# Kernel optimization log

Measured on AMD Instinct MI355X. Metric: run time of the kernel, lower is better.

The kernel has to match this reference:

```python
import jax, jax.numpy as jnp
import numpy as np

# --- dims from Mamba3Config defaults ---
D_MODEL = 768
D_STATE = 192
EXPAND = 2
HEADDIM = 64
D_INNER = EXPAND * D_MODEL        # 1536
NHEADS = D_INNER // HEADDIM       # 24
NGROUPS = 1
NROT = int(D_STATE * 0.5)         # rope_fraction=0.5 -> 96 rotated state dims
NPAIR = NROT // 2                 # 48
A_FLOOR = 1e-4
DT_MIN, DT_MAX = 1e-3, 0.1
EPS = 1e-6
BATCH, SEQ = 1, 1024
D_INPROJ = 2 * D_INNER + 2 * NGROUPS * D_STATE + NHEADS  # 3480


def zcrms(x, scale):
    # Zero-centered RMSNorm: (1 + scale) * RMSNorm(x)
    y = x * jax.lax.rsqrt(jnp.mean(x * x, axis=-1, keepdims=True) + EPS)
    return y * (1.0 + scale)


def _rotate(v, cos, sin):
    # Rotate first NROT state dims in pairs by angle phi (cos/sin: [B,L,H,NPAIR]).
    vr = v[..., :NROT].reshape(v.shape[:-1] + (NPAIR, 2))
    v0, v1 = vr[..., 0], vr[..., 1]
    rot = jnp.stack([v0 * cos - v1 * sin, v0 * sin + v1 * cos], axis=-1)
    return jnp.concatenate([rot.reshape(v.shape[:-1] + (NROT,)), v[..., NROT:]], axis=-1)


def _mamba3(h, W_in, dt_bias, A_log, omega, D, norm_weight, W_out):
    Bsz, L, _ = h.shape
    zxbcdt = h @ W_in  # [B,L,3480]
    z = zxbcdt[..., :D_INNER]
    u = zxbcdt[..., D_INNER:2 * D_INNER].reshape(Bsz, L, NHEADS, HEADDIM)
    Bm = zxbcdt[..., 2 * D_INNER:2 * D_INNER + D_STATE]              # [B,L,N] (ngroups=1)
    Cm = zxbcdt[..., 2 * D_INNER + D_STATE:2 * D_INNER + 2 * D_STATE]
    dt_raw = zxbcdt[..., -NHEADS:]

    dt = jax.nn.softplus(dt_raw + dt_bias)        # [B,L,H]
    A = -(jnp.exp(A_log) + A_FLOOR)               # [H], strictly negative (A_floor)
    a = jnp.exp(dt * A)                           # per-step real decay [B,L,H]

    # Complex-state machinery: data-dependent rotation angle phi_t = cumsum(dt)*omega.
    # y_t = sum_s C e^{i th (Phi_t - Phi_s)} B_s u_s  ==  (C rotated by +Phi_t) . scan of (B rotated by -Phi_s) u_s
    phi = jnp.cumsum(dt, axis=1)[..., None] * omega  # [B,L,H,NPAIR]
    cosp, sinp = jnp.cos(phi), jnp.sin(phi)
    Bh = jnp.broadcast_to(Bm[:, :, None, :], (Bsz, L, NHEADS, D_STATE))
    Ch = jnp.broadcast_to(Cm[:, :, None, :], (Bsz, L, NHEADS, D_STATE))
    Brot = _rotate(Bh, cosp, -sinp)  # e^{-i Phi_s} B_s
    Crot = _rotate(Ch, cosp, sinp)   # e^{+i Phi_t} C_t

    halfdt = 0.5 * dt  # trapezoid weights
    # shifted (t-1) sequences for the trapezoid's previous endpoint
    Bprev = jnp.concatenate([jnp.zeros_like(Brot[:, :1]), Brot[:, :-1]], axis=1)
    uprev = jnp.concatenate([jnp.zeros_like(u[:, :1]), u[:, :-1]], axis=1)

    def step(h_prev, inp):
        a_t, hd_t, B_t, Bp_t, C_t, u_t, up_t = inp
        Bu = jnp.einsum('bhn,bhp->bhpn', B_t, u_t)
        Bu_prev = jnp.einsum('bhn,bhp->bhpn', Bp_t, up_t)
        # exp-trapezoid discretization:
        # h_t = e^{dt A} h_{t-1} + (dt/2) B_t u_t + e^{dt A} (dt/2) B_{t-1} u_{t-1}
        hs = (a_t[..., None, None] * h_prev
              + hd_t[..., None, None] * Bu
              + (a_t * hd_t)[..., None, None] * Bu_prev)
        y = jnp.einsum('bhpn,bhn->bhp', hs, C_t)
        return hs, y

    h0 = jnp.zeros((Bsz, NHEADS, HEADDIM, D_STATE), dtype=h.dtype)
    xs = tuple(jnp.moveaxis(t, 1, 0) for t in (a, halfdt, Brot, Bprev, Crot, u, uprev))
    _, ys = jax.lax.scan(step, h0, xs)
    y = jnp.moveaxis(ys, 0, 1)  # [B,L,H,P]

    y = y + D[None, None, :, None] * u  # skip connection
    y = y.reshape(Bsz, L, D_INNER)
    g = y * jax.nn.silu(z)              # gated
    g = g * jax.lax.rsqrt(jnp.mean(g * g, axis=-1, keepdims=True) + EPS) * norm_weight
    return g @ W_out


def setup_inputs() -> dict:
    key = jax.random.key(0)
    ks = jax.random.split(key, 8)
    x = jax.random.normal(ks[0], (BATCH, SEQ, D_MODEL), jnp.float32)
    W_in = jax.random.normal(ks[1], (D_MODEL, D_INPROJ), jnp.float32) * 0.02
    # dt_bias init so softplus(bias) is in [dt_min, dt_max]
    dtv = jnp.exp(jax.random.uniform(ks[2], (NHEADS,)) * (np.log(DT_MAX) - np.log(DT_MIN)) + np.log(DT_MIN))
    dt_bias = dtv + jnp.log(-jnp.expm1(-dtv))
    A_log = jnp.log(jax.random.uniform(ks[3], (NHEADS,), minval=1.0, maxval=16.0))
    omega = jnp.tile((10000.0 ** (-jnp.arange(NPAIR, dtype=jnp.float32) / NPAIR))[None, :], (NHEADS, 1))
    Dp = 1.0 + 0.1 * jax.random.normal(ks[4], (NHEADS,), jnp.float32)
    norm_weight = jnp.ones((D_INNER,), jnp.float32)
    W_out = jax.random.normal(ks[5], (D_INNER, D_MODEL), jnp.float32) * 0.02
    pre_scale = jnp.zeros((D_MODEL,), jnp.float32)
    post_scale = jnp.zeros((D_MODEL,), jnp.float32)
    return dict(x=x, pre_scale=pre_scale, W_in=W_in, dt_bias=dt_bias, A_log=A_log,
                omega=omega, D=Dp, norm_weight=norm_weight, W_out=W_out, post_scale=post_scale)


def reference(x, pre_scale, W_in, dt_bias, A_log, omega, D, norm_weight, W_out, post_scale):
    residual = x
    h = zcrms(x, pre_scale)
    y = _mamba3(h, W_in, dt_bias, A_log, omega, D, norm_weight, W_out)
    y = zcrms(y, post_scale)
    return residual + y  # dropout=0.0
```

## Files before the change

### kernel.cpp

```cpp
#include <hip/hip_runtime.h>
#include <cstdint>

#define L_SEQ   1024
#define DMODEL  768
#define DINNER  1536
#define NHEADS  24
#define HEADDIM 64
#define DSTATE  192
#define NPAIR   48
#define DPROJ   3480
#define NPADJ   3584
#define NCHUNK  16
#define QCH     64
#define EPSF    1e-6f

typedef __attribute__((ext_vector_type(8))) short short8;
typedef __attribute__((ext_vector_type(4))) float f32x4;

__device__ __forceinline__ unsigned short f2bf(float x) {
  union { float f; uint32_t u; } v; v.f = x;
  uint32_t r = (v.u + 0x7FFFu + ((v.u >> 16) & 1u)) >> 16;
  return (unsigned short)r;
}
__device__ __forceinline__ float bf2f(unsigned short b) {
  union { float f; uint32_t u; } v; v.u = ((uint32_t)b) << 16;
  return v.f;
}

__device__ __forceinline__ float blockReduceSum256(float v, float* red) {
#pragma unroll
  for (int m = 32; m; m >>= 1) v += __shfl_xor(v, m, 64);
  int wid = threadIdx.x >> 6, lane = threadIdx.x & 63;
  if (lane == 0) red[wid] = v;
  __syncthreads();
  float s = red[0] + red[1] + red[2] + red[3];
  __syncthreads();
  return s;
}

__global__ __launch_bounds__(256) void k_cvtw(const float* __restrict__ W,
                                              unsigned short* __restrict__ Wh,
                                              int K, int N, int Npad) {
  __shared__ float tile[32][33];
  int n0 = blockIdx.x * 32, k0 = blockIdx.y * 32;
  int tr = threadIdx.x >> 3, tc4 = (threadIdx.x & 7) << 2;
  const float* wp = W + (size_t)(k0 + tr) * N + n0 + tc4;
  float4 v = make_float4(0.f, 0.f, 0.f, 0.f);
  if (n0 + tc4 + 3 < N) {
    v = *(const float4*)wp;
  } else {
    if (n0 + tc4     < N) v.x = wp[0];
    if (n0 + tc4 + 1 < N) v.y = wp[1];
    if (n0 + tc4 + 2 < N) v.z = wp[2];
    if (n0 + tc4 + 3 < N) v.w = wp[3];
  }
  tile[tr][tc4 + 0] = v.x; tile[tr][tc4 + 1] = v.y;
  tile[tr][tc4 + 2] = v.z; tile[tr][tc4 + 3] = v.w;
  __syncthreads();
  ushort4 oh;
  oh.x = f2bf(tile[tc4 + 0][tr]);
  oh.y = f2bf(tile[tc4 + 1][tr]);
  oh.z = f2bf(tile[tc4 + 2][tr]);
  oh.w = f2bf(tile[tc4 + 3][tr]);
  *(ushort4*)&Wh[(size_t)(n0 + tr) * K + k0 + tc4] = oh;
}

__global__ __launch_bounds__(256) void k_prenorm_dt(const float* __restrict__ x,
                                                    const float* __restrict__ pre_scale,
                                                    const float* __restrict__ W_in,
                                                    unsigned short* __restrict__ hb,
                                                    float* __restrict__ dtr) {
  __shared__ float hs[DMODEL];
  __shared__ float red[4];
  __shared__ float part[NHEADS][8];
  int l = blockIdx.x, tid = threadIdx.x;
  const float* xr = x + (size_t)l * DMODEL;
  float v[3]; float ss = 0.f;
#pragma unroll
  for (int k = 0; k < 3; ++k) { v[k] = xr[tid + k * 256]; ss += v[k] * v[k]; }
  ss = blockReduceSum256(ss, red);
  float r = rsqrtf(ss * (1.f / DMODEL) + EPSF);
#pragma unroll
  for (int k = 0; k < 3; ++k) {
    int i = tid + k * 256;
    float hv = v[k] * r * (1.f + pre_scale[i]);
    hs[i] = hv;
    hb[(size_t)l * DMODEL + i] = f2bf(hv);
  }
  __syncthreads();
  if (tid < 192) {
    int hh = tid >> 3, seg = tid & 7;
    float s = 0.f;
    int k0 = seg * 96;
#pragma unroll 4
    for (int k = k0; k < k0 + 96; ++k)
      s = fmaf(hs[k], W_in[(size_t)k * DPROJ + 3456 + hh], s);
    part[hh][seg] = s;
  }
  __syncthreads();
  if (tid < NHEADS) {
    float s = 0.f;
#pragma unroll
    for (int q = 0; q < 8; ++q) s += part[tid][q];
    dtr[(size_t)l * NHEADS + tid] = s;
  }
}

template<int BM, int BN, int TM, int TN>
__global__ __launch_bounds__(256) void k_gemm_bf16(
    const unsigned short* __restrict__ A,
    const unsigned short* __restrict__ Bt,
    float* __restrict__ C,
    int N, int K, int ldc) {
  __shared__ unsigned short As[BM * 32];
  __shared__ unsigned short Bs[BN * 32];
  const int tid = threadIdx.x;
  const int lane = tid & 63, w = tid >> 6;
  const int wm = (w >> 1) * (TM * 16), wn = (w & 1) * (TN * 16);
  const int bm = blockIdx.y * BM, bn = blockIdx.x * BN;
  const int r15 = lane & 15, kg = lane >> 4;
  f32x4 acc[TM][TN] = {};
  for (int k0 = 0; k0 < K; k0 += 32) {
    __syncthreads();
#pragma unroll
    for (int ch = tid; ch < BM * 4; ch += 256) {
      int r = ch >> 2, kq = (ch & 3) << 3;
      *(short8*)&As[r * 32 + kq] = *(const short8*)&A[(size_t)(bm + r) * K + k0 + kq];
    }
#pragma unroll
    for (int ch = tid; ch < BN * 4; ch += 256) {
      int r = ch >> 2, kq = (ch & 3) << 3;
      *(short8*)&Bs[r * 32 + kq] = *(const short8*)&Bt[(size_t)(bn + r) * K + k0 + kq];
    }
    __syncthreads();
    short8 af[TM], bfr[TN];
#pragma unroll
    for (int i = 0; i < TM; ++i)
      af[i] = *(const short8*)&As[(wm + i * 16 + r15) * 32 + kg * 8];
#pragma unroll
    for (int j = 0; j < TN; ++j)
      bfr[j] = *(const short8*)&Bs[(wn + j * 16 + r15) * 32 + kg * 8];
#pragma unroll
    for (int i = 0; i < TM; ++i)
#pragma unroll
      for (int j = 0; j < TN; ++j)
        acc[i][j] = __builtin_amdgcn_mfma_f32_16x16x32_bf16(af[i], bfr[j], acc[i][j], 0, 0, 0);
  }
  const int crow = bm + wm + (lane >> 4) * 4;
  const int ccol = bn + wn + r15;
#pragma unroll
  for (int i = 0; i < TM; ++i)
#pragma unroll
    for (int j = 0; j < TN; ++j) {
      int col = ccol + j * 16;
      if (col < N) {
        float* cp = C + (size_t)(crow + i * 16) * ldc + col;
#pragma unroll
        for (int r = 0; r < 4; ++r) cp[(size_t)r * ldc] = acc[i][j][r];
      }
    }
}

__global__ __launch_bounds__(256) void k_dtscan(const float* __restrict__ dtr,
                                                const float* __restrict__ dt_bias,
                                                const float* __restrict__ A_log,
                                                float* __restrict__ halfdt,
                                                float* __restrict__ cfac,
                                                float* __restrict__ cumdt,
                                                float* __restrict__ cumD) {
  __shared__ float sdt[L_SEQ];
  __shared__ float wsum[4];
  int hh = blockIdx.x, tid = threadIdx.x;
  int lane = tid & 63, wid = tid >> 6;
  float bias = dt_bias[hh];
  float Ah = -(expf(A_log[hh]) + 1e-4f);
  int l0 = tid * 4;
  float d[4], e[4];
#pragma unroll
  for (int k = 0; k < 4; ++k) {
    float draw = dtr[(size_t)(l0 + k) * NHEADS + hh] + bias;
    d[k] = (draw > 20.f) ? draw : log1pf(expf(draw));
    sdt[l0 + k] = d[k];
  }
  e[0] = d[0]; e[1] = e[0] + d[1]; e[2] = e[1] + d[2]; e[3] = e[2] + d[3];
  float tot = e[3];
  float s = tot;
#pragma unroll
  for (int off = 1; off < 64; off <<= 1) {
    float n = __shfl_up(s, off, 64);
    if (lane >= off) s += n;
  }
  if (lane == 63) wsum[wid] = s;
  __syncthreads();
  float woff = 0.f;
#pragma unroll
  for (int q = 0; q < 4; ++q) woff += (q < wid) ? wsum[q] : 0.f;
  float excl = woff + s - tot;
  float cd0 = excl + e[0], cd1 = excl + e[1], cd2 = excl + e[2], cd3 = excl + e[3];
  float dnext3 = (l0 + 3 < L_SEQ - 1) ? sdt[l0 + 4] : 0.f;
  float4 o_hd = make_float4(0.5f * d[0], 0.5f * d[1], 0.5f * d[2], 0.5f * d[3]);
  float4 o_cf = make_float4(0.5f * (d[0] + d[1]), 0.5f * (d[1] + d[2]),
                            0.5f * (d[2] + d[3]), 0.5f * (d[3] + dnext3));
  float4 o_cd = make_float4(cd0, cd1, cd2, cd3);
  float4 o_cD = make_float4(Ah * cd0, Ah * cd1, Ah * cd2, Ah * cd3);
  size_t idx = (size_t)hh * L_SEQ + l0;
  *(float4*)&halfdt[idx] = o_hd;
  *(float4*)&cfac[idx]   = o_cf;
  *(float4*)&cumdt[idx]  = o_cd;
  *(float4*)&cumD[idx]   = o_cD;
}

__global__ __launch_bounds__(256) void k_rotate(const float* __restrict__ zx,
                                                const float* __restrict__ cumdt,
                                                const float* __restrict__ omega,
                                                unsigned short* __restrict__ Brot,
                                                unsigned short* __restrict__ Crot,
                                                float* __restrict__ U) {
  int l = blockIdx.x, tid = threadIdx.x;
  const float* row = zx + (size_t)l * DPROJ;
  for (int i = tid; i < 384; i += 256) {
    float4 v = *(const float4*)(row + 1536 + i * 4);
    int hh = i >> 4;
    int p = (i & 15) << 2;
    *(float4*)&U[((size_t)(hh * L_SEQ + l)) * HEADDIM + p] = v;
  }
  for (int i = tid; i < NHEADS * 96; i += 256) {
    int hh = i / 96, j = i - hh * 96;
    int n = 2 * j;
    float b0 = row[3072 + n], b1 = row[3072 + n + 1];
    float c0 = row[3264 + n], c1 = row[3264 + n + 1];
    size_t base = ((size_t)(hh * L_SEQ + l)) * DSTATE + n;
    float br0 = b0, br1 = b1, cr0 = c0, cr1 = c1;
    if (j < NPAIR) {
      float ph = cumdt[hh * L_SEQ + l] * omega[hh * NPAIR + j];
      float sp, cp;
      sincosf(ph, &sp, &cp);
      br0 =  b0 * cp + b1 * sp;
      br1 = -b0 * sp + b1 * cp;
      cr0 =  c0 * cp - c1 * sp;
      cr1 =  c0 * sp + c1 * cp;
    }
    ushort2 bo, co;
    bo.x = f2bf(br0); bo.y = f2bf(br1);
    co.x = f2bf(cr0); co.y = f2bf(cr1);
    *(ushort2*)&Brot[base] = bo;
    *(ushort2*)&Crot[base] = co;
  }
}

__global__ __launch_bounds__(256) void k_chunkX(const unsigned short* __restrict__ Brot,
                                                const float* __restrict__ U,
                                                const float* __restrict__ cumD,
                                                const float* __restrict__ cfac,
                                                float* __restrict__ X) {
  const int c = blockIdx.x, hh = blockIdx.y;
  const int tid = threadIdx.x;
  const size_t hl = (size_t)hh * L_SEQ;
  const int l0 = c * QCH;
  __shared__ float Bs[QCH][DSTATE];
  __shared__ float su[QCH][HEADDIM];
  for (int i = tid; i < QCH * 48; i += 256) {
    int m = i / 48, q = i - m * 48;
    ushort4 bv = *(const ushort4*)&Brot[(hl + l0 + m) * DSTATE + (q << 2)];
    Bs[m][(q << 2) + 0] = bf2f(bv.x);
    Bs[m][(q << 2) + 1] = bf2f(bv.y);
    Bs[m][(q << 2) + 2] = bf2f(bv.z);
    Bs[m][(q << 2) + 3] = bf2f(bv.w);
  }
  float dlast = cumD[hl + l0 + QCH - 1];
  for (int i = tid; i < QCH * 16; i += 256) {
    int m = i >> 4, q = i & 15;
    float s = expf(dlast - cumD[hl + l0 + m]) * cfac[hl + l0 + m];
    float4 v = *(const float4*)&U[(hl + l0 + m) * HEADDIM + (q << 2)];
    v.x *= s; v.y *= s; v.z *= s; v.w *= s;
    *(float4*)&su[m][q << 2] = v;
  }
  __syncthreads();
  const int ngrp = tid & 15, pgrp = tid >> 4;
  const int n0 = ngrp * 12, p0 = pgrp << 2;
  float acc[12][4] = {};
  for (int m = 0; m < QCH; ++m) {
    const float4 uv = *(const float4*)&su[m][p0];
    const float4 b0 = *(const float4*)&Bs[m][n0];
    const float4 b1 = *(const float4*)&Bs[m][n0 + 4];
    const float4 b2 = *(const float4*)&Bs[m][n0 + 8];
    float u4[4] = {uv.x, uv.y, uv.z, uv.w};
    float bb[12] = {b0.x, b0.y, b0.z, b0.w, b1.x, b1.y, b1.z, b1.w, b2.x, b2.y, b2.z, b2.w};
#pragma unroll
    for (int j = 0; j < 12; ++j)
#pragma unroll
      for (int i = 0; i < 4; ++i) acc[j][i] = fmaf(bb[j], u4[i], acc[j][i]);
  }
  const size_t obase = ((size_t)(hh * NCHUNK + c)) * (HEADDIM * DSTATE);
#pragma unroll
  for (int i = 0; i < 4; ++i)
#pragma unroll
    for (int j4 = 0; j4 < 3; ++j4)
      *(float4*)&X[obase + (size_t)(p0 + i) * DSTATE + n0 + j4 * 4] =
          make_float4(acc[j4 * 4 + 0][i], acc[j4 * 4 + 1][i], acc[j4 * 4 + 2][i], acc[j4 * 4 + 3][i]);
}

__global__ __launch_bounds__(256) void k_statepass(const float* __restrict__ X,
                                                   const float* __restrict__ cumD,
                                                   unsigned short* __restrict__ Hs) {
  int hh = blockIdx.x >> 3, part = blockIdx.x & 7;
  int tid = threadIdx.x;
  const size_t hl = (size_t)hh * L_SEQ;
  float Hc[6] = {0.f, 0.f, 0.f, 0.f, 0.f, 0.f};
  for (int c = 0; c < NCHUNK; ++c) {
    float r = 1.f;
    if (c > 0) r = expf(cumD[hl + c * QCH + QCH - 1] - cumD[hl + c * QCH - 1]);
    size_t base = ((size_t)(hh * NCHUNK + c)) * (HEADDIM * DSTATE) + part * 1536 + tid;
#pragma unroll
    for (int k = 0; k < 6; ++k) {
      Hs[base + k * 256] = f2bf(Hc[k]);
      Hc[k] = fmaf(r, Hc[k], X[base + k * 256]);
    }
  }
}

#define YP 104
#define SP 72
__global__ __launch_bounds__(256) void k_yout_mfma(
    const unsigned short* __restrict__ Brot, const unsigned short* __restrict__ Crot,
    const float* __restrict__ U,             const unsigned short* __restrict__ Hs,
    const float* __restrict__ cumD, const float* __restrict__ cfac,
    const float* __restrict__ halfdt, const float* __restrict__ Dvec,
    float* __restrict__ Yout) {
  const int c = blockIdx.x, hh = blockIdx.y;
  const int tid = threadIdx.x;
  const int lane = tid & 63, w = tid >> 6;
  const int wr = w >> 1, wc = w & 1;
  const int r15 = lane & 15, kg = lane >> 4;
  const int l0 = c * QCH;
  const size_t hl = (size_t)hh * L_SEQ;

  __shared__ unsigned short Cs[64][YP];
  __shared__ unsigned short Bs[64][YP];
  __shared__ unsigned short Ss[64][SP];
  __shared__ unsigned short Ut[64][SP];
  __shared__ float Dc[64], cfs[64], hds[64];

  if (tid < 64) {
    Dc[tid]  = cumD[hl + l0 + tid];
    cfs[tid] = cfac[hl + l0 + tid];
    hds[tid] = halfdt[hl + l0 + tid];
  }
  for (int idx = tid; idx < 64 * 64; idx += 256) {
    int m = idx >> 6, p = idx & 63;
    Ut[p][m] = f2bf(U[(hl + l0 + m) * HEADDIM + p]);
  }

  f32x4 accS[2][2] = {};
  for (int half = 0; half < 2; ++half) {
    __syncthreads();
    for (int idx = tid; idx < 64 * 12; idx += 256) {
      int t = idx / 12, q = (idx % 12) << 3;
      *(short8*)&Cs[t][q] = *(const short8*)&Crot[(hl + l0 + t) * DSTATE + 96 * half + q];
      *(short8*)&Bs[t][q] = *(const short8*)&Brot[(hl + l0 + t) * DSTATE + 96 * half + q];
    }
    __syncthreads();
#pragma unroll
    for (int kk = 0; kk < 3; ++kk) {
      short8 af[2], bfr[2];
#pragma unroll
      for (int i = 0; i < 2; ++i)
        af[i] = *(const short8*)&Cs[wr * 32 + i * 16 + r15][kk * 32 + kg * 8];
#pragma unroll
      for (int j = 0; j < 2; ++j)
        bfr[j] = *(const short8*)&Bs[wc * 32 + j * 16 + r15][kk * 32 + kg * 8];
#pragma unroll
      for (int i = 0; i < 2; ++i)
#pragma unroll
        for (int j = 0; j < 2; ++j)
          accS[i][j] = __builtin_amdgcn_mfma_f32_16x16x32_bf16(af[i], bfr[j], accS[i][j], 0, 0, 0);
    }
  }
#pragma unroll
  for (int i = 0; i < 2; ++i)
#pragma unroll
    for (int j = 0; j < 2; ++j)
#pragma unroll
      for (int r = 0; r < 4; ++r) {
        int t = wr * 32 + i * 16 + kg * 4 + r;
        int m = wc * 32 + j * 16 + r15;
        float wgt = 0.f;
        if (m < t)       wgt = __expf(Dc[t] - Dc[m]) * cfs[m];
        else if (m == t) wgt = hds[t];
        Ss[t][m] = f2bf(accS[i][j][r] * wgt);
      }

  f32x4 accZ[2][2] = {};
  const size_t hcb = ((size_t)(hh * NCHUNK + c)) * (HEADDIM * DSTATE);
  for (int half = 0; half < 2; ++half) {
    __syncthreads();
    for (int idx = tid; idx < 64 * 12; idx += 256) {
      int t = idx / 12, q = (idx % 12) << 3;
      *(short8*)&Cs[t][q] = *(const short8*)&Crot[(hl + l0 + t) * DSTATE + 96 * half + q];
      *(short8*)&Bs[t][q] = *(const short8*)&Hs[hcb + (size_t)t * DSTATE + 96 * half + q];
    }
    __syncthreads();
#pragma unroll
    for (int kk = 0; kk < 3; ++kk) {
      short8 af[2], bfr[2];
#pragma unroll
      for (int i = 0; i < 2; ++i)
        af[i] = *(const short8*)&Cs[wr * 32 + i * 16 + r15][kk * 32 + kg * 8];
#pragma unroll
      for (int j = 0; j < 2; ++j)
        bfr[j] = *(const short8*)&Bs[wc * 32 + j * 16 + r15][kk * 32 + kg * 8];
#pragma unroll
      for (int i = 0; i < 2; ++i)
#pragma unroll
        for (int j = 0; j < 2; ++j)
          accZ[i][j] = __builtin_amdgcn_mfma_f32_16x16x32_bf16(af[i], bfr[j], accZ[i][j], 0, 0, 0);
    }
  }

  f32x4 accY[2][2] = {};
#pragma unroll
  for (int kk = 0; kk < 2; ++kk) {
    short8 af[2], bfr[2];
#pragma unroll
    for (int i = 0; i < 2; ++i)
      af[i] = *(const short8*)&Ss[wr * 32 + i * 16 + r15][kk * 32 + kg * 8];
#pragma unroll
    for (int j = 0; j < 2; ++j)
      bfr[j] = *(const short8*)&Ut[wc * 32 + j * 16 + r15][kk * 32 + kg * 8];
#pragma unroll
    for (int i = 0; i < 2; ++i)
#pragma unroll
      for (int j = 0; j < 2; ++j)
        accY[i][j] = __builtin_amdgcn_mfma_f32_16x16x32_bf16(af[i], bfr[j], accY[i][j], 0, 0, 0);
  }

  float Dbase = (c > 0) ? cumD[hl + l0 - 1] : 0.f;
  float Dh = Dvec[hh];
#pragma unroll
  for (int i = 0; i < 2; ++i)
#pragma unroll
    for (int r = 0; r < 4; ++r) {
      int t = wr * 32 + i * 16 + kg * 4 + r;
      float et = __expf(Dc[t] - Dbase);
#pragma unroll
      for (int j = 0; j < 2; ++j) {
        int p = wc * 32 + j * 16 + r15;
        float u = U[(hl + l0 + t) * HEADDIM + p];
        Yout[(size_t)(l0 + t) * DINNER + hh * HEADDIM + p] =
            accY[i][j][r] + et * accZ[i][j][r] + Dh * u;
      }
    }
}

__global__ __launch_bounds__(256) void k_gate(const float* __restrict__ Y,
                                              const float* __restrict__ zx,
                                              const float* __restrict__ nw,
                                              unsigned short* __restrict__ Gh) {
  __shared__ float gbuf[DINNER];
  __shared__ float red[4];
  int l = blockIdx.x, tid = threadIdx.x;
  float ss = 0.f;
  for (int i = tid; i < DINNER; i += 256) {
    float y = Y[(size_t)l * DINNER + i];
    float z = zx[(size_t)l * DPROJ + i];
    float g = y * z / (1.f + expf(-z));
    gbuf[i] = g;
    ss += g * g;
  }
  ss = blockReduceSum256(ss, red);
  float r = rsqrtf(ss * (1.f / DINNER) + EPSF);
  for (int i = tid; i < DINNER; i += 256)
    Gh[(size_t)l * DINNER + i] = f2bf(gbuf[i] * r * nw[i]);
}

__global__ __launch_bounds__(256) void k_final(const float* __restrict__ x,
                                               const float* __restrict__ T,
                                               const float* __restrict__ post_scale,
                                               float* __restrict__ out) {
  __shared__ float red[4];
  int l = blockIdx.x, tid = threadIdx.x;
  const float* tr = T + (size_t)l * DMODEL;
  float v[3]; float ss = 0.f;
#pragma unroll
  for (int k = 0; k < 3; ++k) { v[k] = tr[tid + k * 256]; ss += v[k] * v[k]; }
  ss = blockReduceSum256(ss, red);
  float r = rsqrtf(ss * (1.f / DMODEL) + EPSF);
#pragma unroll
  for (int k = 0; k < 3; ++k) {
    int i = tid + k * 256;
    out[(size_t)l * DMODEL + i] = x[(size_t)l * DMODEL + i] + v[k] * r * (1.f + post_scale[i]);
  }
}

extern "C" void kernel_launch(void* const* d_in, const int* in_sizes, int n_in,
                              void* d_out, int out_size, void* d_ws, size_t ws_size,
                              hipStream_t stream) {
  const float* x      = (const float*)d_in[0];
  const float* pre_s  = (const float*)d_in[1];
  const float* W_in   = (const float*)d_in[2];
  const float* dt_b   = (const float*)d_in[3];
  const float* A_log  = (const float*)d_in[4];
  const float* omega  = (const float*)d_in[5];
  const float* Dvec   = (const float*)d_in[6];
  const float* nw     = (const float*)d_in[7];
  const float* W_out  = (const float*)d_in[8];
  const float* post_s = (const float*)d_in[9];
  float* out = (float*)d_out;

  float* ws = (float*)d_ws;
  size_t off = 0;
  auto nxt = [&](size_t n) { float* p = ws + off; off += (n + 3) & ~(size_t)3; return p; };
  float* ws_zx  = nxt((size_t)L_SEQ * DPROJ);
  unsigned short* ws_hb = (unsigned short*)nxt((size_t)L_SEQ * DMODEL / 2);
  float* ws_dtr = nxt((size_t)L_SEQ * NHEADS);
  float* ws_hd  = nxt((size_t)NHEADS * L_SEQ);
  float* ws_cf  = nxt((size_t)NHEADS * L_SEQ);
  float* ws_cdt = nxt((size_t)NHEADS * L_SEQ);
  float* ws_cD  = nxt((size_t)NHEADS * L_SEQ);
  unsigned short* ws_Brb = (unsigned short*)nxt((size_t)NHEADS * L_SEQ * DSTATE / 2);
  unsigned short* ws_Crb = (unsigned short*)nxt((size_t)NHEADS * L_SEQ * DSTATE / 2);
  float* ws_U   = nxt((size_t)NHEADS * L_SEQ * HEADDIM);
  float* ws_X   = nxt((size_t)NHEADS * NCHUNK * HEADDIM * DSTATE);
  unsigned short* ws_Hsb = (unsigned short*)nxt((size_t)NHEADS * NCHUNK * HEADDIM * DSTATE / 2);
  float* ws_Y   = nxt((size_t)L_SEQ * DINNER);
  unsigned short* ws_Gh = (unsigned short*)nxt((size_t)L_SEQ * DINNER / 2);
  unsigned short* ws_W1h = (unsigned short*)ws_X;
  unsigned short* ws_W2h = ws_Brb;
  float* ws_T = ws_X;

  k_cvtw<<<dim3(NPADJ / 32, DMODEL / 32), 256, 0, stream>>>(W_in, ws_W1h, DMODEL, DPROJ, NPADJ);
  k_prenorm_dt<<<L_SEQ, 256, 0, stream>>>(x, pre_s, W_in, ws_hb, ws_dtr);
  k_gemm_bf16<128, 128, 4, 4><<<dim3(NPADJ / 128, L_SEQ / 128), 256, 0, stream>>>(
      ws_hb, ws_W1h, ws_zx, DPROJ, DMODEL, DPROJ);
  k_dtscan<<<NHEADS, 256, 0, stream>>>(ws_dtr, dt_b, A_log, ws_hd, ws_cf, ws_cdt, ws_cD);
  k_rotate<<<L_SEQ, 256, 0, stream>>>(ws_zx, ws_cdt, omega, ws_Brb, ws_Crb, ws_U);
  k_chunkX<<<dim3(NCHUNK, NHEADS), 256, 0, stream>>>(ws_Brb, ws_U, ws_cD, ws_cf, ws_X);
  k_statepass<<<NHEADS * 8, 256, 0, stream>>>(ws_X, ws_cD, ws_Hsb);
  k_yout_mfma<<<dim3(NCHUNK, NHEADS), 256, 0, stream>>>(ws_Brb, ws_Crb, ws_U, ws_Hsb, ws_cD, ws_cf, ws_hd, Dvec, ws_Y);
  k_cvtw<<<dim3(DMODEL / 32, DINNER / 32), 256, 0, stream>>>(W_out, ws_W2h, DINNER, DMODEL, DMODEL);
  k_gate<<<L_SEQ, 256, 0, stream>>>(ws_Y, ws_zx, nw, ws_Gh);
  k_gemm_bf16<64, 64, 2, 2><<<dim3(DMODEL / 64, L_SEQ / 64), 256, 0, stream>>>(
      ws_Gh, ws_W2h, ws_T, DMODEL, DINNER, DMODEL);
  k_final<<<L_SEQ, 256, 0, stream>>>(x, ws_T, post_s, out);
}
```

Before: 218.8 us.

## Merge weight conversions, prefetch GEMM tiles in registers, store U as bf16

Both weight transpose/convert kernels become one launch writing to dedicated workspace buffers, which removes a launch and the aliasing onto scratch. The bf16 GEMM now loads the next K-slice into registers while computing the current one, hiding global load latency at the cost of more registers. The first GEMM's tile shrinks to 128x64 to launch more blocks. U is stored as bf16 instead of fp32, halving its traffic in the scan kernels but losing precision on the D skip term.

```diff
diff --git a/kernel.cpp b/kernel.cpp
--- a/kernel.cpp
+++ b/kernel.cpp
@@ -38,11 +38,20 @@
   return s;
 }
 
-__global__ __launch_bounds__(256) void k_cvtw(const float* __restrict__ W,
-                                              unsigned short* __restrict__ Wh,
-                                              int K, int N, int Npad) {
+__global__ __launch_bounds__(256) void k_cvtw2(const float* __restrict__ Wa,
+                                               unsigned short* __restrict__ Wha,
+                                               const float* __restrict__ Wb,
+                                               unsigned short* __restrict__ Whb) {
   __shared__ float tile[32][33];
-  int n0 = blockIdx.x * 32, k0 = blockIdx.y * 32;
+  int b = blockIdx.x;
+  const float* W; unsigned short* Wt; int K, N, bx, by;
+  if (b < 112 * 24) {
+    W = Wa; Wt = Wha; K = DMODEL; N = DPROJ; bx = b % 112; by = b / 112;
+  } else {
+    b -= 112 * 24;
+    W = Wb; Wt = Whb; K = DINNER; N = DMODEL; bx = b % 24; by = b / 24;
+  }
+  int n0 = bx * 32, k0 = by * 32;
   int tr = threadIdx.x >> 3, tc4 = (threadIdx.x & 7) << 2;
   const float* wp = W + (size_t)(k0 + tr) * N + n0 + tc4;
   float4 v = make_float4(0.f, 0.f, 0.f, 0.f);
@@ -62,7 +71,7 @@
   oh.y = f2bf(tile[tc4 + 1][tr]);
   oh.z = f2bf(tile[tc4 + 2][tr]);
   oh.w = f2bf(tile[tc4 + 3][tr]);
-  *(ushort4*)&Wh[(size_t)(n0 + tr) * K + k0 + tc4] = oh;
+  *(ushort4*)&Wt[(size_t)(n0 + tr) * K + k0 + tc4] = oh;
 }
 
 __global__ __launch_bounds__(256) void k_prenorm_dt(const float* __restrict__ x,
@@ -112,6 +121,8 @@
     const unsigned short* __restrict__ Bt,
     float* __restrict__ C,
     int N, int K, int ldc) {
+  constexpr int AC = (BM * 4) / 256;
+  constexpr int BC = (BN * 4) / 256;
   __shared__ unsigned short As[BM * 32];
   __shared__ unsigned short Bs[BN * 32];
   const int tid = threadIdx.x;
@@ -119,20 +130,34 @@
   const int wm = (w >> 1) * (TM * 16), wn = (w & 1) * (TN * 16);
   const int bm = blockIdx.y * BM, bn = blockIdx.x * BN;
   const int r15 = lane & 15, kg = lane >> 4;
+  short8 ra[AC], rb[BC];
+  auto loadG = [&](int k0) {
+#pragma unroll
+    for (int a = 0; a < AC; ++a) {
+      int idx = tid + a * 256; int r = idx >> 2, kq = (idx & 3) << 3;
+      ra[a] = *(const short8*)&A[(size_t)(bm + r) * K + k0 + kq];
+    }
+#pragma unroll
+    for (int b = 0; b < BC; ++b) {
+      int idx = tid + b * 256; int r = idx >> 2, kq = (idx & 3) << 3;
+      rb[b] = *(const short8*)&Bt[(size_t)(bn + r) * K + k0 + kq];
+    }
+  };
   f32x4 acc[TM][TN] = {};
+  loadG(0);
   for (int k0 = 0; k0 < K; k0 += 32) {
+#pragma unroll
+    for (int a = 0; a < AC; ++a) {
+      int idx = tid + a * 256; int r = idx >> 2, kq = (idx & 3) << 3;
+      *(short8*)&As[r * 32 + kq] = ra[a];
+    }
+#pragma unroll
+    for (int b = 0; b < BC; ++b) {
+      int idx = tid + b * 256; int r = idx >> 2, kq = (idx & 3) << 3;
+      *(short8*)&Bs[r * 32 + kq] = rb[b];
+    }
     __syncthreads();
-#pragma unroll
-    for (int ch = tid; ch < BM * 4; ch += 256) {
-      int r = ch >> 2, kq = (ch & 3) << 3;
-      *(short8*)&As[r * 32 + kq] = *(const short8*)&A[(size_t)(bm + r) * K + k0 + kq];
-    }
-#pragma unroll
-    for (int ch = tid; ch < BN * 4; ch += 256) {
-      int r = ch >> 2, kq = (ch & 3) << 3;
-      *(short8*)&Bs[r * 32 + kq] = *(const short8*)&Bt[(size_t)(bn + r) * K + k0 + kq];
-    }
-    __syncthreads();
+    if (k0 + 32 < K) loadG(k0 + 32);
     short8 af[TM], bfr[TN];
 #pragma unroll
     for (int i = 0; i < TM; ++i)
@@ -145,6 +170,7 @@
 #pragma unroll
       for (int j = 0; j < TN; ++j)
         acc[i][j] = __builtin_amdgcn_mfma_f32_16x16x32_bf16(af[i], bfr[j], acc[i][j], 0, 0, 0);
+    __syncthreads();
   }
   const int crow = bm + wm + (lane >> 4) * 4;
   const int ccol = bn + wn + r15;
@@ -215,14 +241,16 @@
                                                 const float* __restrict__ omega,
                                                 unsigned short* __restrict__ Brot,
                                                 unsigned short* __restrict__ Crot,
-                                                float* __restrict__ U) {
+                                                unsigned short* __restrict__ Ub) {
   int l = blockIdx.x, tid = threadIdx.x;
   const float* row = zx + (size_t)l * DPROJ;
   for (int i = tid; i < 384; i += 256) {
     float4 v = *(const float4*)(row + 1536 + i * 4);
     int hh = i >> 4;
     int p = (i & 15) << 2;
-    *(float4*)&U[((size_t)(hh * L_SEQ + l)) * HEADDIM + p] = v;
+    ushort4 o;
+    o.x = f2bf(v.x); o.y = f2bf(v.y); o.z = f2bf(v.z); o.w = f2bf(v.w);
+    *(ushort4*)&Ub[((size_t)(hh * L_SEQ + l)) * HEADDIM + p] = o;
   }
   for (int i = tid; i < NHEADS * 96; i += 256) {
     int hh = i / 96, j = i - hh * 96;
@@ -249,7 +277,7 @@
 }
 
 __global__ __launch_bounds__(256) void k_chunkX(const unsigned short* __restrict__ Brot,
-                                                const float* __restrict__ U,
+                                                const unsigned short* __restrict__ Ub,
                                                 const float* __restrict__ cumD,
                                                 const float* __restrict__ cfac,
                                                 float* __restrict__ X) {
@@ -271,8 +299,10 @@
   for (int i = tid; i < QCH * 16; i += 256) {
     int m = i >> 4, q = i & 15;
     float s = expf(dlast - cumD[hl + l0 + m]) * cfac[hl + l0 + m];
-    float4 v = *(const float4*)&U[(hl + l0 + m) * HEADDIM + (q << 2)];
-    v.x *= s; v.y *= s; v.z *= s; v.w *= s;
+    ushort4 uv = *(const ushort4*)&Ub[(hl + l0 + m) * HEADDIM + (q << 2)];
+    float4 v;
+    v.x = bf2f(uv.x) * s; v.y = bf2f(uv.y) * s;
+    v.z = bf2f(uv.z) * s; v.w = bf2f(uv.w) * s;
     *(float4*)&su[m][q << 2] = v;
   }
   __syncthreads();
@@ -323,7 +353,7 @@
 #define SP 72
 __global__ __launch_bounds__(256) void k_yout_mfma(
     const unsigned short* __restrict__ Brot, const unsigned short* __restrict__ Crot,
-    const float* __restrict__ U,             const unsigned short* __restrict__ Hs,
+    const unsigned short* __restrict__ Ub,   const unsigned short* __restrict__ Hs,
     const float* __restrict__ cumD, const float* __restrict__ cfac,
     const float* __restrict__ halfdt, const float* __restrict__ Dvec,
     float* __restrict__ Yout) {
@@ -348,7 +378,7 @@
   }
   for (int idx = tid; idx < 64 * 64; idx += 256) {
     int m = idx >> 6, p = idx & 63;
-    Ut[p][m] = f2bf(U[(hl + l0 + m) * HEADDIM + p]);
+    Ut[p][m] = Ub[(hl + l0 + m) * HEADDIM + p];
   }
 
   f32x4 accS[2][2] = {};
@@ -445,7 +475,7 @@
 #pragma unroll
       for (int j = 0; j < 2; ++j) {
         int p = wc * 32 + j * 16 + r15;
-        float u = U[(hl + l0 + t) * HEADDIM + p];
+        float u = bf2f(Ub[(hl + l0 + t) * HEADDIM + p]);
         Yout[(size_t)(l0 + t) * DINNER + hh * HEADDIM + p] =
             accY[i][j][r] + et * accZ[i][j][r] + Dh * u;
       }
@@ -519,25 +549,24 @@
   float* ws_cD  = nxt((size_t)NHEADS * L_SEQ);
   unsigned short* ws_Brb = (unsigned short*)nxt((size_t)NHEADS * L_SEQ * DSTATE / 2);
   unsigned short* ws_Crb = (unsigned short*)nxt((size_t)NHEADS * L_SEQ * DSTATE / 2);
-  float* ws_U   = nxt((size_t)NHEADS * L_SEQ * HEADDIM);
+  unsigned short* ws_Ub  = (unsigned short*)nxt((size_t)NHEADS * L_SEQ * HEADDIM / 2);
   float* ws_X   = nxt((size_t)NHEADS * NCHUNK * HEADDIM * DSTATE);
   unsigned short* ws_Hsb = (unsigned short*)nxt((size_t)NHEADS * NCHUNK * HEADDIM * DSTATE / 2);
   float* ws_Y   = nxt((size_t)L_SEQ * DINNER);
-  unsigned short* ws_Gh = (unsigned short*)nxt((size_t)L_SEQ * DINNER / 2);
-  unsigned short* ws_W1h = (unsigned short*)ws_X;
-  unsigned short* ws_W2h = ws_Brb;
+  unsigned short* ws_Gh  = (unsigned short*)nxt((size_t)L_SEQ * DINNER / 2);
+  unsigned short* ws_W1h = (unsigned short*)nxt((size_t)NPADJ * DMODEL / 2);
+  unsigned short* ws_W2h = (unsigned short*)nxt((size_t)DMODEL * DINNER / 2);
   float* ws_T = ws_X;
 
-  k_cvtw<<<dim3(NPADJ / 32, DMODEL / 32), 256, 0, stream>>>(W_in, ws_W1h, DMODEL, DPROJ, NPADJ);
+  k_cvtw2<<<112 * 24 + 24 * 48, 256, 0, stream>>>(W_in, ws_W1h, W_out, ws_W2h);
   k_prenorm_dt<<<L_SEQ, 256, 0, stream>>>(x, pre_s, W_in, ws_hb, ws_dtr);
-  k_gemm_bf16<128, 128, 4, 4><<<dim3(NPADJ / 128, L_SEQ / 128), 256, 0, stream>>>(
+  k_gemm_bf16<128, 64, 4, 2><<<dim3(NPADJ / 64, L_SEQ / 128), 256, 0, stream>>>(
       ws_hb, ws_W1h, ws_zx, DPROJ, DMODEL, DPROJ);
   k_dtscan<<<NHEADS, 256, 0, stream>>>(ws_dtr, dt_b, A_log, ws_hd, ws_cf, ws_cdt, ws_cD);
-  k_rotate<<<L_SEQ, 256, 0, stream>>>(ws_zx, ws_cdt, omega, ws_Brb, ws_Crb, ws_U);
-  k_chunkX<<<dim3(NCHUNK, NHEADS), 256, 0, stream>>>(ws_Brb, ws_U, ws_cD, ws_cf, ws_X);
+  k_rotate<<<L_SEQ, 256, 0, stream>>>(ws_zx, ws_cdt, omega, ws_Brb, ws_Crb, ws_Ub);
+  k_chunkX<<<dim3(NCHUNK, NHEADS), 256, 0, stream>>>(ws_Brb, ws_Ub, ws_cD, ws_cf, ws_X);
   k_statepass<<<NHEADS * 8, 256, 0, stream>>>(ws_X, ws_cD, ws_Hsb);
-  k_yout_mfma<<<dim3(NCHUNK, NHEADS), 256, 0, stream>>>(ws_Brb, ws_Crb, ws_U, ws_Hsb, ws_cD, ws_cf, ws_hd, Dvec, ws_Y);
-  k_cvtw<<<dim3(DMODEL / 32, DINNER / 32), 256, 0, stream>>>(W_out, ws_W2h, DINNER, DMODEL, DMODEL);
+  k_yout_mfma<<<dim3(NCHUNK, NHEADS), 256, 0, stream>>>(ws_Brb, ws_Crb, ws_Ub, ws_Hsb, ws_cD, ws_cf, ws_hd, Dvec, ws_Y);
   k_gate<<<L_SEQ, 256, 0, stream>>>(ws_Y, ws_zx, nw, ws_Gh);
   k_gemm_bf16<64, 64, 2, 2><<<dim3(DMODEL / 64, L_SEQ / 64), 256, 0, stream>>>(
       ws_Gh, ws_W2h, ws_T, DMODEL, DINNER, DMODEL);
```

Measured after the change: 199.0 us. 9.0% less time.
